# Optimization experiments

Measured on AMD Instinct MI355X. Metric: run time of the kernel, lower is better.

## Reference

```python
import jax, jax.numpy as jnp
import numpy as np

B, S, D = 64, 512, 1024   # batch, max_phon_seq_len, d_model
V = 64                    # phonological vocabulary size
T = 131072                # total ragged tokens (avg 4 per (batch, position) slot)


def setup_inputs() -> dict:
    key = jax.random.key(0)
    k1, k2, k3, k4 = jax.random.split(key, 4)
    tokens = jax.random.randint(k1, (T,), 0, V)                      # flat token indices
    segment_ids = jnp.sort(jax.random.randint(k2, (T,), 0, B * S))   # sorted segment id per token
    phon_embedding = jax.random.normal(k3, (V, D), dtype=jnp.float32)
    phon_pos_embedding = jax.random.normal(k4, (S, D), dtype=jnp.float32)
    return {
        "tokens": tokens,
        "segment_ids": segment_ids,
        "phon_embedding": phon_embedding,
        "phon_pos_embedding": phon_pos_embedding,
    }


def reference(tokens, segment_ids, phon_embedding, phon_pos_embedding):
    # Fused ragged segment-mean embedding (EmbeddingBag 'mean' semantics):
    # for each (batch, position) segment, mean of embeddings of its tokens.
    gathered = phon_embedding[tokens]                                   # [T, D]
    sums = jax.ops.segment_sum(gathered, segment_ids, num_segments=B * S)          # [B*S, D]
    counts = jax.ops.segment_sum(jnp.ones((T,), dtype=gathered.dtype),
                                 segment_ids, num_segments=B * S)       # [B*S]
    means = sums / jnp.maximum(counts, 1.0)[:, None]                    # empty slots stay zero
    # add positional embedding, as in embed_phon_tokens
    out = means.reshape(B, S, D) + phon_pos_embedding[None, :, :]       # [B, S, D]
    return out
```

## Files before the change

kernel.cpp:

```cpp
#include <hip/hip_runtime.h>
#include <hip/hip_bf16.h>

#define BB 64
#define SS 512
#define DD 1024
#define NSEG (BB * SS)

typedef float floatx4 __attribute__((ext_vector_type(4)));

__global__ __launch_bounds__(256) void fill_bounds_kernel(
    const int* __restrict__ seg_ids,
    int* __restrict__ seg_start,
    int T)
{
    int t = blockIdx.x * blockDim.x + threadIdx.x;
    if (t >= T) return;
    int cur  = seg_ids[t];
    int prev = (t == 0) ? -1 : seg_ids[t - 1];
    for (int s = prev + 1; s <= cur; ++s) seg_start[s] = t;
    if (t == T - 1) {
        for (int s = cur + 1; s <= NSEG; ++s) seg_start[s] = T;
    }
}

__global__ __launch_bounds__(256) void seg_mean_embed_kernel(
    const int* __restrict__ tokens,
    const int* __restrict__ seg_start,
    const float* __restrict__ emb,
    const float* __restrict__ pos,
    float* __restrict__ out)
{
    const int seg = blockIdx.x;
    const int lo = seg_start[seg];
    const int hi = seg_start[seg + 1];

    const int d = threadIdx.x * 4;

    floatx4 acc = (floatx4)(0.f);
    for (int t = lo; t < hi; ++t) {
        const int tok = tokens[t];
        const floatx4 v = *reinterpret_cast<const floatx4*>(emb + (size_t)tok * DD + d);
        acc += v;
    }

    const int cnt = hi - lo;
    const float inv = (cnt > 0) ? (1.0f / (float)cnt) : 0.0f;

    const int s = seg & (SS - 1);
    const floatx4 p = *reinterpret_cast<const floatx4*>(pos + (size_t)s * DD + d);

    floatx4 o = acc * inv + p;

    *reinterpret_cast<floatx4*>(out + (size_t)seg * DD + d) = o;
}

__device__ __forceinline__ int lower_bound_dev(const int* __restrict__ a, int n, int key) {
    int lo = 0, hi = n;
    while (lo < hi) {
        int mid = (lo + hi) >> 1;
        if (a[mid] < key) lo = mid + 1; else hi = mid;
    }
    return lo;
}

__global__ __launch_bounds__(256) void seg_mean_embed_bsearch_kernel(
    const int* __restrict__ tokens,
    const int* __restrict__ seg_ids,
    const float* __restrict__ emb,
    const float* __restrict__ pos,
    float* __restrict__ out,
    int T)
{
    const int seg = blockIdx.x;
    const int lo = lower_bound_dev(seg_ids, T, seg);
    const int hi = lower_bound_dev(seg_ids, T, seg + 1);
    const int d = threadIdx.x * 4;

    floatx4 acc = (floatx4)(0.f);
    for (int t = lo; t < hi; ++t) {
        const int tok = tokens[t];
        const floatx4 v = *reinterpret_cast<const floatx4*>(emb + (size_t)tok * DD + d);
        acc += v;
    }
    const int cnt = hi - lo;
    const float inv = (cnt > 0) ? (1.0f / (float)cnt) : 0.0f;
    const int s = seg & (SS - 1);
    const floatx4 p = *reinterpret_cast<const floatx4*>(pos + (size_t)s * DD + d);
    floatx4 o = acc * inv + p;
    *reinterpret_cast<floatx4*>(out + (size_t)seg * DD + d) = o;
}

extern "C" void kernel_launch(void* const* d_in, const int* in_sizes, int n_in,
                              void* d_out, int out_size, void* d_ws, size_t ws_size,
                              hipStream_t stream) {
    const int*   tokens  = (const int*)d_in[0];
    const int*   seg_ids = (const int*)d_in[1];
    const float* emb     = (const float*)d_in[2];
    const float* pos     = (const float*)d_in[3];
    float*       out     = (float*)d_out;
    const int T = in_sizes[0];

    const size_t need = (size_t)(NSEG + 1) * sizeof(int);
    if (ws_size >= need) {
        int* seg_start = (int*)d_ws;
        fill_bounds_kernel<<<(T + 255) / 256, 256, 0, stream>>>(seg_ids, seg_start, T);
        seg_mean_embed_kernel<<<NSEG, 256, 0, stream>>>(tokens, seg_start, emb, pos, out);
    } else {
        seg_mean_embed_bsearch_kernel<<<NSEG, 256, 0, stream>>>(tokens, seg_ids, emb, pos, out, T);
    }
}
```

Before: 43.14 us.

## Assign one wavefront per segment with multi-chunk accumulation and nontemporal stores

Restructures the main kernel so each 64-lane wavefront handles one whole segment: every lane accumulates four float4 chunks across the embedding row, and eight segments share a 512-thread block. This removes per-segment block launch overhead and cross-wave redundancy in loading segment bounds and token indices. The positional row is loaded before the token loop so its latency overlaps the gather. Output is written with nontemporal stores to avoid polluting cache with the large output. The cost is more registers per lane and less parallelism for latency hiding within one segment.

```diff
diff --git a/kernel.cpp b/kernel.cpp
--- a/kernel.cpp
+++ b/kernel.cpp
@@ -4,9 +4,13 @@
 #define BB 64
 #define SS 512
 #define DD 1024
+#define VV 64
 #define NSEG (BB * SS)
+#define THREADS 512
+#define WPB (THREADS / 64)
+#define GRID (NSEG / WPB)
 
-typedef float floatx4 __attribute__((ext_vector_type(4)));
+typedef float f32x4 __attribute__((ext_vector_type(4)));
 
 __global__ __launch_bounds__(256) void fill_bounds_kernel(
     const int* __restrict__ seg_ids,
@@ -23,35 +27,50 @@
     }
 }
 
-__global__ __launch_bounds__(256) void seg_mean_embed_kernel(
+__global__ __launch_bounds__(THREADS) void seg_mean_wps_kernel(
     const int* __restrict__ tokens,
     const int* __restrict__ seg_start,
     const float* __restrict__ emb,
     const float* __restrict__ pos,
     float* __restrict__ out)
 {
-    const int seg = blockIdx.x;
+    const int wave = threadIdx.x >> 6;
+    const int lane = threadIdx.x & 63;
+    const int seg  = blockIdx.x * WPB + wave;
+    const int d0   = lane * 4;
+
     const int lo = seg_start[seg];
     const int hi = seg_start[seg + 1];
 
-    const int d = threadIdx.x * 4;
+    const float* prow = pos + (size_t)(seg & (SS - 1)) * DD + d0;
+    f32x4 p0 = *reinterpret_cast<const f32x4*>(prow);
+    f32x4 p1 = *reinterpret_cast<const f32x4*>(prow + 256);
+    f32x4 p2 = *reinterpret_cast<const f32x4*>(prow + 512);
+    f32x4 p3 = *reinterpret_cast<const f32x4*>(prow + 768);
 
-    floatx4 acc = (floatx4)(0.f);
+    f32x4 a0 = (f32x4)(0.f), a1 = (f32x4)(0.f), a2 = (f32x4)(0.f), a3 = (f32x4)(0.f);
     for (int t = lo; t < hi; ++t) {
         const int tok = tokens[t];
-        const floatx4 v = *reinterpret_cast<const floatx4*>(emb + (size_t)tok * DD + d);
-        acc += v;
+        const float* erow = emb + (size_t)tok * DD + d0;
+        a0 += *reinterpret_cast<const f32x4*>(erow);
+        a1 += *reinterpret_cast<const f32x4*>(erow + 256);
+        a2 += *reinterpret_cast<const f32x4*>(erow + 512);
+        a3 += *reinterpret_cast<const f32x4*>(erow + 768);
     }
 
     const int cnt = hi - lo;
     const float inv = (cnt > 0) ? (1.0f / (float)cnt) : 0.0f;
 
-    const int s = seg & (SS - 1);
-    const floatx4 p = *reinterpret_cast<const floatx4*>(pos + (size_t)s * DD + d);
+    f32x4 o0 = a0 * inv + p0;
+    f32x4 o1 = a1 * inv + p1;
+    f32x4 o2 = a2 * inv + p2;
+    f32x4 o3 = a3 * inv + p3;
 
-    floatx4 o = acc * inv + p;
-
-    *reinterpret_cast<floatx4*>(out + (size_t)seg * DD + d) = o;
+    float* orow = out + (size_t)seg * DD + d0;
+    __builtin_nontemporal_store(o0, reinterpret_cast<f32x4*>(orow));
+    __builtin_nontemporal_store(o1, reinterpret_cast<f32x4*>(orow + 256));
+    __builtin_nontemporal_store(o2, reinterpret_cast<f32x4*>(orow + 512));
+    __builtin_nontemporal_store(o3, reinterpret_cast<f32x4*>(orow + 768));
 }
 
 __device__ __forceinline__ int lower_bound_dev(const int* __restrict__ a, int n, int key) {
@@ -76,18 +95,17 @@
     const int hi = lower_bound_dev(seg_ids, T, seg + 1);
     const int d = threadIdx.x * 4;
 
-    floatx4 acc = (floatx4)(0.f);
+    f32x4 acc = (f32x4)(0.f);
     for (int t = lo; t < hi; ++t) {
         const int tok = tokens[t];
-        const floatx4 v = *reinterpret_cast<const floatx4*>(emb + (size_t)tok * DD + d);
-        acc += v;
+        acc += *reinterpret_cast<const f32x4*>(emb + (size_t)tok * DD + d);
     }
     const int cnt = hi - lo;
     const float inv = (cnt > 0) ? (1.0f / (float)cnt) : 0.0f;
     const int s = seg & (SS - 1);
-    const floatx4 p = *reinterpret_cast<const floatx4*>(pos + (size_t)s * DD + d);
-    floatx4 o = acc * inv + p;
-    *reinterpret_cast<floatx4*>(out + (size_t)seg * DD + d) = o;
+    const f32x4 p = *reinterpret_cast<const f32x4*>(pos + (size_t)s * DD + d);
+    f32x4 o = acc * inv + p;
+    *reinterpret_cast<f32x4*>(out + (size_t)seg * DD + d) = o;
 }
 
 extern "C" void kernel_launch(void* const* d_in, const int* in_sizes, int n_in,
@@ -104,7 +122,7 @@
     if (ws_size >= need) {
         int* seg_start = (int*)d_ws;
         fill_bounds_kernel<<<(T + 255) / 256, 256, 0, stream>>>(seg_ids, seg_start, T);
-        seg_mean_embed_kernel<<<NSEG, 256, 0, stream>>>(tokens, seg_start, emb, pos, out);
+        seg_mean_wps_kernel<<<GRID, THREADS, 0, stream>>>(tokens, seg_start, emb, pos, out);
     } else {
         seg_mean_embed_bsearch_kernel<<<NSEG, 256, 0, stream>>>(tokens, seg_ids, emb, pos, out, T);
     }
```

New measurement: 40.26 us. -6.7%, faster.
